# Kernel tuning notes

Hardware: AMD Instinct MI355X
Metric: run time of the kernel (lower is better)

Reference implementation:

```python
import jax, jax.numpy as jnp
import numpy as np

P = 8.0  # Lp norm order for NormDist layers (finite-p distance conv)
CHUNK = 8  # output-channel chunk for memory-bounded distance computation
EPS = 8.0 / 255.0


def lp_norm(d, p=P):
    # stable Lp norm over last axis: m * (sum((d/m)^p))^(1/p)
    m = jnp.max(d, axis=-1)
    ms = jnp.where(m > 0, m, 1.0)
    s = jnp.sum((d / ms[..., None]) ** p, axis=-1)
    ss = jnp.where(m > 0, s, 1.0)
    return m * ss ** (1.0 / p)


def extract_patches(t, k, s, pad):
    # [B,C,H,W] -> [B, L, C*k*k] (torch-unfold channel-major ordering), L=Ho*Wo
    pt = jax.lax.conv_general_dilated_patches(t, (k, k), (s, s), [(pad, pad), (pad, pad)])
    B, F, Ho, Wo = pt.shape
    return pt.reshape(B, F, Ho * Wo).transpose(0, 2, 1), Ho, Wo


def normdist_conv(c, lo, hi, w, k, s, pad):
    # Lp-distance conv with interval bound propagation on (center, lower, upper)
    pc, Ho, Wo = extract_patches(c, k, s, pad)
    pl, _, _ = extract_patches(lo, k, s, pad)
    ph, _, _ = extract_patches(hi, k, s, pad)
    O = w.shape[0]
    wf = w.reshape(O, -1)  # [O, F]

    def per_chunk(wc):  # wc: [CHUNK, F]
        dc = jnp.abs(pc[:, :, None, :] - wc)                     # [B,L,CHUNK,F]
        oc = lp_norm(dc)
        # per-element distance bounds given lo <= x <= hi
        dl = jnp.maximum(jnp.maximum(pl[:, :, None, :] - wc, wc - ph[:, :, None, :]), 0.0)
        ol = lp_norm(dl)
        dh = jnp.maximum(jnp.abs(pl[:, :, None, :] - wc), jnp.abs(ph[:, :, None, :] - wc))
        oh = lp_norm(dh)
        return oc, ol, oh

    oc, ol, oh = jax.lax.map(per_chunk, wf.reshape(O // CHUNK, CHUNK, -1))

    def to_img(t):  # [nch, B, L, CHUNK] -> [B, O, Ho, Wo]
        nch, B, L, ch = t.shape
        return t.transpose(1, 0, 3, 2).reshape(B, nch * ch, Ho, Wo)

    return to_img(oc), to_img(ol), to_img(oh)


def bound_relu(c, lo, hi):
    return jax.nn.relu(c), jax.nn.relu(lo), jax.nn.relu(hi)


def _mp(t):
    return jax.lax.reduce_window(t, -jnp.inf, jax.lax.max, (1, 1, 3, 3), (1, 1, 2, 2), 'VALID')


def bound_maxpool(c, lo, hi):
    return _mp(c), _mp(lo), _mp(hi)


def bound_linear(c, lo, hi, W, b=None):
    oc = c @ W.T
    mid = ((lo + hi) * 0.5) @ W.T
    rad = ((hi - lo) * 0.5) @ jnp.abs(W).T
    if b is not None:
        oc = oc + b
        mid = mid + b
    return oc, mid - rad, mid + rad


def setup_inputs() -> dict:
    key = jax.random.key(0)
    ks = jax.random.split(key, 10)
    x = jax.random.normal(ks[0], (16, 3, 32, 32), jnp.float32)
    lower = x - EPS
    upper = x + EPS
    w1 = jax.random.normal(ks[1], (96, 3, 7, 7), jnp.float32)
    w2 = jax.random.normal(ks[2], (256, 96, 5, 5), jnp.float32)
    w3 = jax.random.normal(ks[3], (384, 256, 3, 3), jnp.float32)
    w4 = jax.random.normal(ks[4], (384, 384, 3, 3), jnp.float32)
    w5 = jax.random.normal(ks[5], (256, 384, 3, 3), jnp.float32)
    fw1 = jax.random.normal(ks[6], (1024, 2304), jnp.float32) * 0.02
    fw2 = jax.random.normal(ks[7], (512, 1024), jnp.float32) * 0.03
    fw3 = jax.random.normal(ks[8], (10, 512), jnp.float32) * 0.04
    fb3 = jax.random.normal(ks[9], (10,), jnp.float32)
    return {"x": x, "lower": lower, "upper": upper, "w1": w1, "w2": w2, "w3": w3,
            "w4": w4, "w5": w5, "fw1": fw1, "fw2": fw2, "fw3": fw3, "fb3": fb3}


def reference(x, lower, upper, w1, w2, w3, w4, w5, fw1, fw2, fw3, fb3):
    c, l, u = normdist_conv(x, lower, upper, w1, 7, 2, 2)   # 32 -> 15
    c, l, u = bound_relu(c, l, u)
    c, l, u = bound_maxpool(c, l, u)                        # 15 -> 7
    c, l, u = normdist_conv(c, l, u, w2, 5, 1, 2)           # 7 -> 7
    c, l, u = bound_relu(c, l, u)
    c, l, u = bound_maxpool(c, l, u)                        # 7 -> 3
    c, l, u = normdist_conv(c, l, u, w3, 3, 1, 1)
    c, l, u = bound_relu(c, l, u)
    c, l, u = normdist_conv(c, l, u, w4, 3, 1, 1)
    c, l, u = bound_relu(c, l, u)
    c, l, u = normdist_conv(c, l, u, w5, 3, 1, 1)
    c, l, u = bound_relu(c, l, u)
    B = c.shape[0]
    c, l, u = c.reshape(B, -1), l.reshape(B, -1), u.reshape(B, -1)
    c, l, u = bound_linear(c, l, u, fw1)
    c, l, u = bound_relu(c, l, u)
    c, l, u = bound_linear(c, l, u, fw2)
    c, l, u = bound_relu(c, l, u)
    c, l, u = bound_linear(c, l, u, fw3, fb3)
    # final negation swaps the roles of lower/upper
    return (-c, -u, -l)
```

## Files before the change

kernel.cpp:

```cpp
#include <hip/hip_runtime.h>
#include <math.h>


typedef float vf2 __attribute__((ext_vector_type(2)));

__device__ __forceinline__ float rt8(float s) { return sqrtf(sqrtf(sqrtf(s))); }

__device__ __forceinline__ void tap16(float w, float pc, float pl, float pu,
                                      float& aC, float& aL, float& aH)
{
    float a = pc - w; float a2 = a * a, a4 = a2 * a2; aC = fmaf(a4, a4, aC);
    float x = pl - w, y = pu - w;
    float dl = fmaxf(fmaxf(x, -y), 0.f);
    float e2 = dl * dl, e4 = e2 * e2; aL = fmaf(e4, e4, aL);
    float h2 = fmaxf(x * x, y * y);
    float h4 = h2 * h2; aH = fmaf(h4, h4, aH);
}

__device__ __forceinline__ void tap16v2(vf2 w, vf2 pc, vf2 pl, vf2 pu,
                                        vf2& aC, vf2& aL, vf2& aH)
{
    vf2 a = pc - w; vf2 a2 = a * a, a4 = a2 * a2;
    aC = __builtin_elementwise_fma(a4, a4, aC);
    vf2 x = pl - w, y = pu - w;
    vf2 zero = {0.f, 0.f};
    vf2 dl = __builtin_elementwise_max(__builtin_elementwise_max(x, -y), zero);
    vf2 e2 = dl * dl, e4 = e2 * e2;
    aL = __builtin_elementwise_fma(e4, e4, aL);
    vf2 h2 = __builtin_elementwise_max(x * x, y * y);
    vf2 h4 = h2 * h2;
    aH = __builtin_elementwise_fma(h4, h4, aH);
}

__launch_bounds__(256)
__global__ void wtrans4(const float* __restrict__ W2, const float* __restrict__ W3,
                        const float* __restrict__ W4, const float* __restrict__ W5,
                        float* __restrict__ T2, float* __restrict__ T3,
                        float* __restrict__ T4, float* __restrict__ T5)
{
    constexpr int nt2 = 4 * 38, nt3 = 6 * 36, nt4 = 6 * 54, nt5 = 4 * 54;
    int bid = blockIdx.x;
    const float* W; float* T; int O, CK, KK, t;
    if (bid < nt2)                   { W = W2; T = T2; O = 256; CK = 2400; KK = 25; t = bid; }
    else if (bid < nt2 + nt3)        { W = W3; T = T3; O = 384; CK = 2304; KK = 9; t = bid - nt2; }
    else if (bid < nt2 + nt3 + nt4)  { W = W4; T = T4; O = 384; CK = 3456; KK = 9; t = bid - nt2 - nt3; }
    else                             { W = W5; T = T5; O = 256; CK = 3456; KK = 9; t = bid - nt2 - nt3 - nt4; }
    int tilesC = (CK + 63) / 64;
    int to = t / tilesC, tc = t - to * tilesC;
    int o0 = to * 64, c0 = tc * 64;
    __shared__ float tile[64][65];
    int lane = threadIdx.x & 63, wv = threadIdx.x >> 6;
    #pragma unroll
    for (int i = 0; i < 16; ++i) {
        int row = wv + i * 4;
        int c = c0 + lane;
        tile[row][lane] = (c < CK) ? W[(size_t)(o0 + row) * CK + c] : 0.f;
    }
    __syncthreads();
    #pragma unroll
    for (int i = 0; i < 16; ++i) {
        int row = wv + i * 4;
        int ck = c0 + row;
        if (ck < CK) {
            int c = ck / KK, tt = ck - c * KK;
            T[(size_t)((c >> 1) * KK + tt) * (2 * O) + (size_t)(o0 + lane) * 2 + (c & 1)]
                = tile[lane][row];
        }
    }
}

template<int K, int S, int PAD, int CC, int HIN, int WIN, int HO, int WO>
__launch_bounds__(256)
__global__ void conv_a(const float* __restrict__ IC, const float* __restrict__ IL,
                       const float* __restrict__ IU, const float* __restrict__ W,
                       float* __restrict__ OUT, int B, int Cin, int O, int OG)
{
    constexpr int PH = (HO - 1) * S + K;
    constexpr int PW = (WO - 1) * S + K;
    constexpr int PP = PH * PW;
    constexpr int HW = HIN * WIN;
    constexpr int NP = HO * WO;
    constexpr int ROUNDS = (NP + 63) / 64;
    __shared__ float lds[CC * 3 * PP];

    int og = blockIdx.x % OG;
    int b  = (blockIdx.x / OG) % B;
    int tid = threadIdx.x;

    for (int i = tid; i < CC * 3 * PP; i += 256) lds[i] = 0.f;
    __syncthreads();
    for (int tsel = 0; tsel < 3; ++tsel) {
        const float* src = (tsel == 0 ? IC : (tsel == 1 ? IL : IU))
                         + (size_t)b * Cin * HW;
        for (int e = tid; e < CC * HW; e += 256) {
            int c = e / HW, p = e % HW;
            int pr = p / WIN, pw_ = p % WIN;
            lds[c * 3 * PP + tsel * PP + (pr + PAD) * PW + (pw_ + PAD)] = src[e];
        }
    }
    __syncthreads();

    int wave = tid >> 6, lane = tid & 63;
    int o = __builtin_amdgcn_readfirstlane(og * 4 + wave);
    const float* wp = W + (size_t)o * Cin * (K * K);

    for (int r = 0; r < ROUNDS; ++r) {
        int pos = r * 64 + lane;
        bool act = pos < NP;
        int pp = act ? pos : 0;
        int oh = pp / WO, ow = pp % WO;
        const float* sl = lds + (oh * S) * PW + ow * S;
        const float* wc = wp;
        float aC = 0.f, aL = 0.f, aH = 0.f;
        for (int c = 0; c < CC; ++c) {
            #pragma unroll
            for (int kh = 0; kh < K; ++kh)
                #pragma unroll
                for (int kw = 0; kw < K; ++kw) {
                    float w = wc[kh * K + kw];
                    tap16(w, sl[kh * PW + kw], sl[PP + kh * PW + kw],
                          sl[2 * PP + kh * PW + kw], aC, aL, aH);
                }
            sl += 3 * PP; wc += K * K;
        }
        if (act) {
            size_t N = (size_t)B * O * NP;
            size_t oidx = ((size_t)b * O + o) * NP + pos;
            OUT[oidx] = aC; OUT[N + oidx] = aL; OUT[2 * N + oidx] = aH;
        }
    }
}

__global__ void pool_rt8(const float* __restrict__ in, float* __restrict__ out,
                         int BC, int Hin, int Win, int Ho, int Wo,
                         int n_in, int n_out)
{
    int idx = blockIdx.x * blockDim.x + threadIdx.x;
    int per = BC * Ho * Wo;
    if (idx >= 3 * per) return;
    int tsel = idx / per; int r = idx - tsel * per;
    int ow = r % Wo; int t2 = r / Wo;
    int oh = t2 % Ho; int bc = t2 / Ho;
    const float* ip = in + (size_t)tsel * n_in + (size_t)bc * Hin * Win;
    int ih0 = oh * 2, iw0 = ow * 2;
    float m = -INFINITY;
    #pragma unroll
    for (int i = 0; i < 3; ++i)
        #pragma unroll
        for (int j = 0; j < 3; ++j)
            m = fmaxf(m, ip[(ih0 + i) * Win + (iw0 + j)]);
    out[(size_t)tsel * n_out + r] = rt8(m);
}

template<int CC>
__launch_bounds__(256)
__global__ void conv2_kernel(const float* __restrict__ IN, const float* __restrict__ WT,
                             float* __restrict__ P, int nin)
{
    constexpr int B = 16, Cin = 96, O = 256;
    constexpr int CP = CC / 2;
    constexpr size_t N = (size_t)B * O * 49;
    __shared__ __align__(16) float slab[CP * 360];
    int x = blockIdx.x;
    int oh   = x % 7;
    int b    = (x / 7) % B;
    int chunk = x / (7 * B);
    int c0 = chunk * CC;
    int tid = threadIdx.x;

    for (int i = tid; i < CP * 360; i += 256) {
        int cp = i / 360; int rem = i - cp * 360;
        int tsel = rem / 120; int rr = rem - tsel * 120;
        int r = rr / 24; int cpar = rr - r * 24;
        int col = cpar >> 1, par = cpar & 1;
        int c = c0 + cp * 2 + par;
        int ih = oh + r - 2, iw = col - 2;
        float v = 0.f;
        if (col < 11 && (unsigned)ih < 7u && (unsigned)iw < 7u)
            v = IN[(size_t)tsel * nin + ((size_t)b * Cin + c) * 49 + ih * 7 + iw];
        slab[i] = v;
    }
    __syncthreads();

    int o = tid;
    vf2 aC2[7], aL2[7], aH2[7];
    vf2 zero = {0.f, 0.f};
    #pragma unroll
    for (int u = 0; u < 7; ++u) { aC2[u] = zero; aL2[u] = zero; aH2[u] = zero; }

    for (int cp = 0; cp < CP; ++cp) {
        const float* wp = WT + (size_t)((c0 / 2 + cp) * 25) * (2 * O) + 2 * o;
        const float* sb = slab + cp * 360;
        #pragma unroll
        for (int r = 0; r < 5; ++r) {
            vf2 wr[5];
            #pragma unroll
            for (int kw = 0; kw < 5; ++kw)
                wr[kw] = *(const vf2*)(wp + (size_t)(r * 5 + kw) * (2 * O));
            vf2 X[12], L[12], U[12];
            #pragma unroll
            for (int i2 = 0; i2 < 12; ++i2) {
                X[i2] = *(const vf2*)(sb + r * 24 + i2 * 2);
                L[i2] = *(const vf2*)(sb + 120 + r * 24 + i2 * 2);
                U[i2] = *(const vf2*)(sb + 240 + r * 24 + i2 * 2);
            }
            #pragma unroll
            for (int ow = 0; ow < 7; ++ow)
                #pragma unroll
                for (int kw = 0; kw < 5; ++kw)
                    tap16v2(wr[kw], X[ow + kw], L[ow + kw], U[ow + kw],
                            aC2[ow], aL2[ow], aH2[ow]);
        }
    }

    float* Pc = P + (size_t)chunk * 3 * N;
    size_t rowbase = ((size_t)(b * 7 + oh) * 7) * O + o;
    #pragma unroll
    for (int u = 0; u < 7; ++u) {
        Pc[rowbase + (size_t)u * O]         = aC2[u].x + aC2[u].y;
        Pc[N + rowbase + (size_t)u * O]     = aL2[u].x + aL2[u].y;
        Pc[2 * N + rowbase + (size_t)u * O] = aH2[u].x + aH2[u].y;
    }
}

__global__ void comb2_pool2(const float* __restrict__ P, float* __restrict__ D)
{
    constexpr int B = 16, O = 256, NCH = 16;
    constexpr size_t N = (size_t)B * O * 49;
    int idx = blockIdx.x * blockDim.x + threadIdx.x;
    if (idx >= 3 * B * 9 * O) return;
    int o = idx & 255; int t = idx >> 8;
    int pos = t % 9; t /= 9;
    int b = t % B; int tsel = t / B;
    int ph = pos / 3, pw = pos % 3;
    float m = 0.f;
    #pragma unroll
    for (int i = 0; i < 3; ++i)
        #pragma unroll
        for (int j = 0; j < 3; ++j) {
            int sp = (ph * 2 + i) * 7 + (pw * 2 + j);
            size_t base = (size_t)tsel * N + ((size_t)b * 49 + sp) * O + o;
            float s = 0.f;
            #pragma unroll
            for (int ch = 0; ch < NCH; ++ch) s += P[(size_t)ch * 3 * N + base];
            m = fmaxf(m, s);
        }
    D[idx] = rt8(m);
}

template<int CC>
__launch_bounds__(384)
__global__ void conv3x3_kernel(const float* __restrict__ IN, const float* __restrict__ WT,
                               float* __restrict__ P, int B, int Cin, int O)
{
    constexpr int CP = CC / 2;
    __shared__ __align__(8) float slab[CP * 150];
    int x = blockIdx.x;
    int b = x % B;
    int chunk = x / B;
    int c0 = chunk * CC;
    int tid = threadIdx.x;

    for (int i = tid; i < CP * 150; i += blockDim.x) {
        int cp = i / 150; int rem = i - cp * 150;
        int tsel = rem / 50; int rr = rem - tsel * 50;
        int p = rr >> 1, par = rr & 1;
        int iy = p / 5, ix = p - iy * 5;
        int ih = iy - 1, iw = ix - 1;
        int c = c0 + cp * 2 + par;
        float v = 0.f;
        if ((unsigned)ih < 3u && (unsigned)iw < 3u)
            v = IN[(((size_t)tsel * B + b) * 9 + (ih * 3 + iw)) * Cin + c];
        slab[i] = v;
    }
    __syncthreads();

    int o = tid;
    vf2 aC2[9], aL2[9], aH2[9];
    vf2 zero = {0.f, 0.f};
    #pragma unroll
    for (int u = 0; u < 9; ++u) { aC2[u] = zero; aL2[u] = zero; aH2[u] = zero; }

    for (int cp = 0; cp < CP; ++cp) {
        const float* wp = WT + (size_t)((c0 / 2 + cp) * 9) * (2 * O) + 2 * o;
        vf2 w2[9];
        #pragma unroll
        for (int t = 0; t < 9; ++t) w2[t] = *(const vf2*)(wp + (size_t)t * (2 * O));
        const float* sb = slab + cp * 150;
        #pragma unroll
        for (int py = 0; py < 3; ++py)
            #pragma unroll
            for (int px = 0; px < 3; ++px)
                #pragma unroll
                for (int ky = 0; ky < 3; ++ky)
                    #pragma unroll
                    for (int kx = 0; kx < 3; ++kx) {
                        int p = (py + ky) * 5 + (px + kx);
                        tap16v2(w2[ky * 3 + kx],
                                *(const vf2*)(sb + p * 2),
                                *(const vf2*)(sb + 50 + p * 2),
                                *(const vf2*)(sb + 100 + p * 2),
                                aC2[py * 3 + px], aL2[py * 3 + px], aH2[py * 3 + px]);
                    }
    }

    size_t N = (size_t)B * O * 9;
    float* Pc = P + (size_t)chunk * 3 * N;
    size_t base = ((size_t)b * 9) * O + o;
    #pragma unroll
    for (int u = 0; u < 9; ++u) {
        Pc[base + (size_t)u * O]         = aC2[u].x + aC2[u].y;
        Pc[N + base + (size_t)u * O]     = aL2[u].x + aL2[u].y;
        Pc[2 * N + base + (size_t)u * O] = aH2[u].x + aH2[u].y;
    }
}

__global__ void conv_comb_flat(const float* __restrict__ P, float* __restrict__ OUT,
                               size_t N3, int NCH)
{
    size_t idx = (size_t)blockIdx.x * blockDim.x + threadIdx.x;
    if (idx >= N3) return;
    float s = 0.f;
    for (int ch = 0; ch < NCH; ++ch) s += P[(size_t)ch * N3 + idx];
    OUT[idx] = rt8(s);
}

__global__ void comb5_std(const float* __restrict__ P, float* __restrict__ G, int NCH)
{
    constexpr int B = 16, O = 256;
    constexpr size_t N = (size_t)B * O * 9;
    size_t idx = (size_t)blockIdx.x * blockDim.x + threadIdx.x;
    if (idx >= 3 * N) return;
    float s = 0.f;
    for (int ch = 0; ch < NCH; ++ch) s += P[(size_t)ch * 3 * N + idx];
    int o = (int)(idx % O); size_t t = idx / O;
    int pos = (int)(t % 9); t /= 9;
    int b = (int)(t % B); int tsel = (int)(t / B);
    G[(size_t)tsel * N + ((size_t)b * O + o) * 9 + pos] = rt8(s);
}

__launch_bounds__(256)
__global__ void fc_gemv(const float* __restrict__ IC, const float* __restrict__ IL,
                        const float* __restrict__ IU, const float* __restrict__ W,
                        float* __restrict__ OUT, int B, int In, int Out)
{
    int gw = (int)((blockIdx.x * blockDim.x + threadIdx.x) >> 6);
    int lane = threadIdx.x & 63;
    if (gw >= B * Out) return;
    int o = gw % Out, b = gw / Out;
    const float4* wr = (const float4*)(W  + (size_t)o * In);
    const float4* cr = (const float4*)(IC + (size_t)b * In);
    const float4* lr = (const float4*)(IL + (size_t)b * In);
    const float4* ur = (const float4*)(IU + (size_t)b * In);
    int In4 = In >> 2;
    float sc = 0.f, sm = 0.f, sr = 0.f;
    for (int i = lane; i < In4; i += 64) {
        float4 w4 = wr[i], c4 = cr[i], l4 = lr[i], u4 = ur[i];
        sc = fmaf(c4.x, w4.x, sc); sc = fmaf(c4.y, w4.y, sc);
        sc = fmaf(c4.z, w4.z, sc); sc = fmaf(c4.w, w4.w, sc);
        sm = fmaf((l4.x + u4.x) * 0.5f, w4.x, sm);
        sm = fmaf((l4.y + u4.y) * 0.5f, w4.y, sm);
        sm = fmaf((l4.z + u4.z) * 0.5f, w4.z, sm);
        sm = fmaf((l4.w + u4.w) * 0.5f, w4.w, sm);
        sr = fmaf((u4.x - l4.x) * 0.5f, fabsf(w4.x), sr);
        sr = fmaf((u4.y - l4.y) * 0.5f, fabsf(w4.y), sr);
        sr = fmaf((u4.z - l4.z) * 0.5f, fabsf(w4.z), sr);
        sr = fmaf((u4.w - l4.w) * 0.5f, fabsf(w4.w), sr);
    }
    #pragma unroll
    for (int off = 32; off; off >>= 1) {
        sc += __shfl_xor(sc, off);
        sm += __shfl_xor(sm, off);
        sr += __shfl_xor(sr, off);
    }
    if (lane == 0) {
        size_t N = (size_t)B * Out;
        size_t idx = (size_t)b * Out + o;
        OUT[idx]         = fmaxf(sc, 0.f);
        OUT[N + idx]     = fmaxf(sm - sr, 0.f);
        OUT[2 * N + idx] = fmaxf(sm + sr, 0.f);
    }
}

__global__ void bound_linear_kernel(
    const float* __restrict__ IC, const float* __restrict__ IL, const float* __restrict__ IU,
    const float* __restrict__ W, const float* __restrict__ bias,
    float* __restrict__ OC, float* __restrict__ OL, float* __restrict__ OU,
    int B, int In, int Out)
{
    int idx = blockIdx.x * blockDim.x + threadIdx.x;
    if (idx >= B * Out) return;
    int o = idx % Out, b = idx / Out;
    const float* wr = W  + (size_t)o * In;
    const float* cr = IC + (size_t)b * In;
    const float* lr = IL + (size_t)b * In;
    const float* ur = IU + (size_t)b * In;
    float sc = 0.f, sm = 0.f, sr = 0.f;
    for (int i = 0; i < In; ++i) {
        float w = wr[i];
        sc = fmaf(cr[i], w, sc);
        sm = fmaf((lr[i] + ur[i]) * 0.5f, w, sm);
        sr = fmaf((ur[i] - lr[i]) * 0.5f, fabsf(w), sr);
    }
    float bb = bias[o]; sc += bb; sm += bb;
    OC[idx] = -sc; OL[idx] = -(sm - sr); OU[idx] = -(sm + sr);
}

extern "C" void kernel_launch(void* const* d_in, const int* in_sizes, int n_in,
                              void* d_out, int out_size, void* d_ws, size_t ws_size,
                              hipStream_t stream)
{
    const float* x   = (const float*)d_in[0];
    const float* lo  = (const float*)d_in[1];
    const float* hi  = (const float*)d_in[2];
    const float* w1  = (const float*)d_in[3];
    const float* w2  = (const float*)d_in[4];
    const float* w3  = (const float*)d_in[5];
    const float* w4  = (const float*)d_in[6];
    const float* w5  = (const float*)d_in[7];
    const float* fw1 = (const float*)d_in[8];
    const float* fw2 = (const float*)d_in[9];
    const float* fw3 = (const float*)d_in[10];
    const float* fb3 = (const float*)d_in[11];
    float* out = (float*)d_out;
    float* ws  = (float*)d_ws;

    const size_t n_c1 = 16u * 96 * 15 * 15;
    const size_t n_p1 = 16u * 96 * 7 * 7;
    const size_t n_d  = 16u * 256 * 9;
    const size_t n_c3 = 16u * 384 * 9;
    const size_t n_c5 = 16u * 256 * 9;
    const size_t n_f1 = 16u * 1024;
    const size_t n_f2 = 16u * 512;

    float* A   = ws;
    float* Bp  = A  + 3 * n_c1;
    float* D   = Bp + 3 * n_p1;
    float* E   = D  + 3 * n_d;
    float* F   = E  + 3 * n_c3;
    float* G   = F  + 3 * n_c3;
    float* H   = G  + 3 * n_c5;
    float* I   = H  + 3 * n_f1;
    float* WT2 = I  + 3 * n_f2;
    float* WT3 = WT2 + 614400;
    float* WT4 = WT3 + 884736;
    float* WT5 = WT4 + 1327104;
    float* SP  = WT5 + 884736;

    const int BS = 256;
    auto grid = [](size_t tot) { return dim3((unsigned)((tot + 255) / 256)); };

    wtrans4<<<4 * 38 + 6 * 36 + 6 * 54 + 4 * 54, BS, 0, stream>>>(
        w2, w3, w4, w5, WT2, WT3, WT4, WT5);

    conv_a<7, 2, 2, 3, 32, 32, 15, 15><<<384, BS, 0, stream>>>(
        x, lo, hi, w1, A, 16, 3, 96, 24);
    pool_rt8<<<grid(3 * n_p1), BS, 0, stream>>>(
        A, Bp, 16 * 96, 15, 15, 7, 7, (int)n_c1, (int)n_p1);
    conv2_kernel<6><<<16 * 16 * 7, 256, 0, stream>>>(Bp, WT2, SP, (int)n_p1);
    comb2_pool2<<<grid(3 * n_d), BS, 0, stream>>>(SP, D);
    conv3x3_kernel<8><<<32 * 16, 384, 0, stream>>>(D, WT3, SP, 16, 256, 384);
    conv_comb_flat<<<grid(3 * n_c3), BS, 0, stream>>>(SP, E, 3 * n_c3, 32);
    conv3x3_kernel<8><<<48 * 16, 384, 0, stream>>>(E, WT4, SP, 16, 384, 384);
    conv_comb_flat<<<grid(3 * n_c3), BS, 0, stream>>>(SP, F, 3 * n_c3, 48);
    conv3x3_kernel<8><<<48 * 16, 256, 0, stream>>>(F, WT5, SP, 16, 384, 256);
    comb5_std<<<grid(3 * n_c5), BS, 0, stream>>>(SP, G, 48);
    fc_gemv<<<grid(16384u * 64), BS, 0, stream>>>(
        G, G + n_c5, G + 2 * n_c5, fw1, H, 16, 2304, 1024);
    fc_gemv<<<grid(8192u * 64), BS, 0, stream>>>(
        H, H + n_f1, H + 2 * n_f1, fw2, I, 16, 1024, 512);
    bound_linear_kernel<<<grid(160), BS, 0, stream>>>(
        I, I + n_f2, I + 2 * n_f2, fw3, fb3,
        out, out + 320, out + 160, 16, 512, 10);
}
```

Measured before the change: 593.6 us.

## Fuse weight transpose with conv1, and fold pooling and partial-sum reductions into consumers

New measurement: 582.5 us. No clear change (-1.9%).

```diff
diff --git a/kernel.cpp b/kernel.cpp
--- a/kernel.cpp
+++ b/kernel.cpp
@@ -33,133 +33,102 @@
 }
 
 __launch_bounds__(256)
-__global__ void wtrans4(const float* __restrict__ W2, const float* __restrict__ W3,
-                        const float* __restrict__ W4, const float* __restrict__ W5,
-                        float* __restrict__ T2, float* __restrict__ T3,
-                        float* __restrict__ T4, float* __restrict__ T5)
-{
-    constexpr int nt2 = 4 * 38, nt3 = 6 * 36, nt4 = 6 * 54, nt5 = 4 * 54;
+__global__ void prep_kernel(const float* __restrict__ W2, const float* __restrict__ W3,
+                            const float* __restrict__ W4, const float* __restrict__ W5,
+                            float* __restrict__ T2, float* __restrict__ T3,
+                            float* __restrict__ T4, float* __restrict__ T5,
+                            const float* __restrict__ IC, const float* __restrict__ IL,
+                            const float* __restrict__ IU, const float* __restrict__ W1,
+                            float* __restrict__ A)
+{
+    constexpr int nt2 = 152, nt3 = 216, nt4 = 324, nt5 = 216;
+    constexpr int NTW = nt2 + nt3 + nt4 + nt5;
+    __shared__ float u[3 * 3 * 1225];
     int bid = blockIdx.x;
-    const float* W; float* T; int O, CK, KK, t;
-    if (bid < nt2)                   { W = W2; T = T2; O = 256; CK = 2400; KK = 25; t = bid; }
-    else if (bid < nt2 + nt3)        { W = W3; T = T3; O = 384; CK = 2304; KK = 9; t = bid - nt2; }
-    else if (bid < nt2 + nt3 + nt4)  { W = W4; T = T4; O = 384; CK = 3456; KK = 9; t = bid - nt2 - nt3; }
-    else                             { W = W5; T = T5; O = 256; CK = 3456; KK = 9; t = bid - nt2 - nt3 - nt4; }
-    int tilesC = (CK + 63) / 64;
-    int to = t / tilesC, tc = t - to * tilesC;
-    int o0 = to * 64, c0 = tc * 64;
-    __shared__ float tile[64][65];
-    int lane = threadIdx.x & 63, wv = threadIdx.x >> 6;
-    #pragma unroll
-    for (int i = 0; i < 16; ++i) {
-        int row = wv + i * 4;
-        int c = c0 + lane;
-        tile[row][lane] = (c < CK) ? W[(size_t)(o0 + row) * CK + c] : 0.f;
-    }
-    __syncthreads();
-    #pragma unroll
-    for (int i = 0; i < 16; ++i) {
-        int row = wv + i * 4;
-        int ck = c0 + row;
-        if (ck < CK) {
-            int c = ck / KK, tt = ck - c * KK;
-            T[(size_t)((c >> 1) * KK + tt) * (2 * O) + (size_t)(o0 + lane) * 2 + (c & 1)]
-                = tile[lane][row];
-        }
-    }
-}
-
-template<int K, int S, int PAD, int CC, int HIN, int WIN, int HO, int WO>
-__launch_bounds__(256)
-__global__ void conv_a(const float* __restrict__ IC, const float* __restrict__ IL,
-                       const float* __restrict__ IU, const float* __restrict__ W,
-                       float* __restrict__ OUT, int B, int Cin, int O, int OG)
-{
-    constexpr int PH = (HO - 1) * S + K;
-    constexpr int PW = (WO - 1) * S + K;
-    constexpr int PP = PH * PW;
-    constexpr int HW = HIN * WIN;
-    constexpr int NP = HO * WO;
-    constexpr int ROUNDS = (NP + 63) / 64;
-    __shared__ float lds[CC * 3 * PP];
-
-    int og = blockIdx.x % OG;
-    int b  = (blockIdx.x / OG) % B;
     int tid = threadIdx.x;
 
-    for (int i = tid; i < CC * 3 * PP; i += 256) lds[i] = 0.f;
+    if (bid < NTW) {
+        const float* W; float* T; int O, CK, KK, t;
+        if (bid < nt2)                  { W = W2; T = T2; O = 256; CK = 2400; KK = 25; t = bid; }
+        else if (bid < nt2 + nt3)       { W = W3; T = T3; O = 384; CK = 2304; KK = 9; t = bid - nt2; }
+        else if (bid < nt2 + nt3 + nt4) { W = W4; T = T4; O = 384; CK = 3456; KK = 9; t = bid - nt2 - nt3; }
+        else                            { W = W5; T = T5; O = 256; CK = 3456; KK = 9; t = bid - nt2 - nt3 - nt4; }
+        int tilesC = (CK + 63) / 64;
+        int to = t / tilesC, tc = t - to * tilesC;
+        int o0 = to * 64, c0 = tc * 64;
+        int lane = tid & 63, wv = tid >> 6;
+        #pragma unroll
+        for (int i = 0; i < 16; ++i) {
+            int row = wv + i * 4;
+            int c = c0 + lane;
+            u[row * 65 + lane] = (c < CK) ? W[(size_t)(o0 + row) * CK + c] : 0.f;
+        }
+        __syncthreads();
+        #pragma unroll
+        for (int i = 0; i < 16; ++i) {
+            int row = wv + i * 4;
+            int ck = c0 + row;
+            if (ck < CK) {
+                int c = ck / KK, tt = ck - c * KK;
+                T[(size_t)((c >> 1) * KK + tt) * (2 * O) + (size_t)(o0 + lane) * 2 + (c & 1)]
+                    = u[lane * 65 + row];
+            }
+        }
+        return;
+    }
+
+    constexpr int PP = 1225, PW = 35, HW = 1024;
+    int t = bid - NTW;
+    int og = t % 24; t /= 24;
+    int b  = t % 16; int r = t / 16;
+
+    for (int i = tid; i < 3 * 3 * PP; i += 256) u[i] = 0.f;
     __syncthreads();
     for (int tsel = 0; tsel < 3; ++tsel) {
-        const float* src = (tsel == 0 ? IC : (tsel == 1 ? IL : IU))
-                         + (size_t)b * Cin * HW;
-        for (int e = tid; e < CC * HW; e += 256) {
+        const float* src = (tsel == 0 ? IC : (tsel == 1 ? IL : IU)) + (size_t)b * 3 * HW;
+        for (int e = tid; e < 3 * HW; e += 256) {
             int c = e / HW, p = e % HW;
-            int pr = p / WIN, pw_ = p % WIN;
-            lds[c * 3 * PP + tsel * PP + (pr + PAD) * PW + (pw_ + PAD)] = src[e];
+            int pr = p / 32, pw_ = p % 32;
+            u[c * 3 * PP + tsel * PP + (pr + 2) * PW + (pw_ + 2)] = src[e];
         }
     }
     __syncthreads();
 
     int wave = tid >> 6, lane = tid & 63;
-    int o = __builtin_amdgcn_readfirstlane(og * 4 + wave);
-    const float* wp = W + (size_t)o * Cin * (K * K);
-
-    for (int r = 0; r < ROUNDS; ++r) {
-        int pos = r * 64 + lane;
-        bool act = pos < NP;
-        int pp = act ? pos : 0;
-        int oh = pp / WO, ow = pp % WO;
-        const float* sl = lds + (oh * S) * PW + ow * S;
-        const float* wc = wp;
+    int o = og * 4 + wave;
+    const float* wp = W1 + (size_t)o * 147;
+    int pos = r * 64 + lane;
+    if (pos < 225) {
+        int oh = pos / 15, ow = pos % 15;
+        const float* sl = u + (oh * 2) * PW + ow * 2;
         float aC = 0.f, aL = 0.f, aH = 0.f;
-        for (int c = 0; c < CC; ++c) {
-            #pragma unroll
-            for (int kh = 0; kh < K; ++kh)
+        #pragma unroll
+        for (int c = 0; c < 3; ++c) {
+            #pragma unroll
+            for (int kh = 0; kh < 7; ++kh)
                 #pragma unroll
-                for (int kw = 0; kw < K; ++kw) {
-                    float w = wc[kh * K + kw];
+                for (int kw = 0; kw < 7; ++kw) {
+                    float w = wp[c * 49 + kh * 7 + kw];
                     tap16(w, sl[kh * PW + kw], sl[PP + kh * PW + kw],
                           sl[2 * PP + kh * PW + kw], aC, aL, aH);
                 }
-            sl += 3 * PP; wc += K * K;
-        }
-        if (act) {
-            size_t N = (size_t)B * O * NP;
-            size_t oidx = ((size_t)b * O + o) * NP + pos;
-            OUT[oidx] = aC; OUT[N + oidx] = aL; OUT[2 * N + oidx] = aH;
-        }
-    }
-}
-
-__global__ void pool_rt8(const float* __restrict__ in, float* __restrict__ out,
-                         int BC, int Hin, int Win, int Ho, int Wo,
-                         int n_in, int n_out)
-{
-    int idx = blockIdx.x * blockDim.x + threadIdx.x;
-    int per = BC * Ho * Wo;
-    if (idx >= 3 * per) return;
-    int tsel = idx / per; int r = idx - tsel * per;
-    int ow = r % Wo; int t2 = r / Wo;
-    int oh = t2 % Ho; int bc = t2 / Ho;
-    const float* ip = in + (size_t)tsel * n_in + (size_t)bc * Hin * Win;
-    int ih0 = oh * 2, iw0 = ow * 2;
-    float m = -INFINITY;
-    #pragma unroll
-    for (int i = 0; i < 3; ++i)
-        #pragma unroll
-        for (int j = 0; j < 3; ++j)
-            m = fmaxf(m, ip[(ih0 + i) * Win + (iw0 + j)]);
-    out[(size_t)tsel * n_out + r] = rt8(m);
+            sl += 3 * PP;
+        }
+        size_t N = (size_t)16 * 96 * 225;
+        size_t oi = ((size_t)b * 96 + o) * 225 + pos;
+        A[oi] = aC; A[N + oi] = aL; A[2 * N + oi] = aH;
+    }
 }
 
 template<int CC>
 __launch_bounds__(256)
-__global__ void conv2_kernel(const float* __restrict__ IN, const float* __restrict__ WT,
-                             float* __restrict__ P, int nin)
+__global__ void conv2_kernel(const float* __restrict__ A, const float* __restrict__ WT,
+                             float* __restrict__ P)
 {
     constexpr int B = 16, Cin = 96, O = 256;
     constexpr int CP = CC / 2;
     constexpr size_t N = (size_t)B * O * 49;
+    constexpr size_t NA = (size_t)B * 96 * 225;
     __shared__ __align__(16) float slab[CP * 360];
     int x = blockIdx.x;
     int oh   = x % 7;
@@ -176,8 +145,17 @@
         int c = c0 + cp * 2 + par;
         int ih = oh + r - 2, iw = col - 2;
         float v = 0.f;
-        if (col < 11 && (unsigned)ih < 7u && (unsigned)iw < 7u)
-            v = IN[(size_t)tsel * nin + ((size_t)b * Cin + c) * 49 + ih * 7 + iw];
+        if (col < 11 && (unsigned)ih < 7u && (unsigned)iw < 7u) {
+            const float* ap = A + (size_t)tsel * NA + ((size_t)b * 96 + c) * 225
+                            + (ih * 2) * 15 + iw * 2;
+            float m = 0.f;
+            #pragma unroll
+            for (int pi = 0; pi < 3; ++pi)
+                #pragma unroll
+                for (int pj = 0; pj < 3; ++pj)
+                    m = fmaxf(m, ap[pi * 15 + pj]);
+            v = rt8(m);
+        }
         slab[i] = v;
     }
     __syncthreads();
@@ -248,7 +226,7 @@
     D[idx] = rt8(m);
 }
 
-template<int CC>
+template<int CC, int NCHIN>
 __launch_bounds__(384)
 __global__ void conv3x3_kernel(const float* __restrict__ IN, const float* __restrict__ WT,
                                float* __restrict__ P, int B, int Cin, int O)
@@ -261,6 +239,7 @@
     int c0 = chunk * CC;
     int tid = threadIdx.x;
 
+    size_t NN = (size_t)B * Cin * 9;
     for (int i = tid; i < CP * 150; i += blockDim.x) {
         int cp = i / 150; int rem = i - cp * 150;
         int tsel = rem / 50; int rr = rem - tsel * 50;
@@ -269,8 +248,17 @@
         int ih = iy - 1, iw = ix - 1;
         int c = c0 + cp * 2 + par;
         float v = 0.f;
-        if ((unsigned)ih < 3u && (unsigned)iw < 3u)
-            v = IN[(((size_t)tsel * B + b) * 9 + (ih * 3 + iw)) * Cin + c];
+        if ((unsigned)ih < 3u && (unsigned)iw < 3u) {
+            size_t base = (size_t)tsel * NN + ((size_t)b * 9 + (ih * 3 + iw)) * Cin + c;
+            if (NCHIN == 0) {
+                v = IN[base];
+            } else {
+                float s = 0.f;
+                #pragma unroll 8
+                for (int ch = 0; ch < NCHIN; ++ch) s += IN[(size_t)ch * 3 * NN + base];
+                v = rt8(s);
+            }
+        }
         slab[i] = v;
     }
     __syncthreads();
@@ -313,16 +301,6 @@
         Pc[N + base + (size_t)u * O]     = aL2[u].x + aL2[u].y;
         Pc[2 * N + base + (size_t)u * O] = aH2[u].x + aH2[u].y;
     }
-}
-
-__global__ void conv_comb_flat(const float* __restrict__ P, float* __restrict__ OUT,
-                               size_t N3, int NCH)
-{
-    size_t idx = (size_t)blockIdx.x * blockDim.x + threadIdx.x;
-    if (idx >= N3) return;
-    float s = 0.f;
-    for (int ch = 0; ch < NCH; ++ch) s += P[(size_t)ch * N3 + idx];
-    OUT[idx] = rt8(s);
 }
 
 __global__ void comb5_std(const float* __restrict__ P, float* __restrict__ G, int NCH)
@@ -425,46 +403,38 @@
     float* out = (float*)d_out;
     float* ws  = (float*)d_ws;
 
-    const size_t n_c1 = 16u * 96 * 15 * 15;
-    const size_t n_p1 = 16u * 96 * 7 * 7;
+    const size_t n_c1 = 16u * 96 * 225;
     const size_t n_d  = 16u * 256 * 9;
-    const size_t n_c3 = 16u * 384 * 9;
     const size_t n_c5 = 16u * 256 * 9;
     const size_t n_f1 = 16u * 1024;
     const size_t n_f2 = 16u * 512;
+    const size_t N3   = 16u * 384 * 9;
 
     float* A   = ws;
-    float* Bp  = A  + 3 * n_c1;
-    float* D   = Bp + 3 * n_p1;
-    float* E   = D  + 3 * n_d;
-    float* F   = E  + 3 * n_c3;
-    float* G   = F  + 3 * n_c3;
+    float* D   = A  + 3 * n_c1;
+    float* G   = D  + 3 * n_d;
     float* H   = G  + 3 * n_c5;
     float* I   = H  + 3 * n_f1;
     float* WT2 = I  + 3 * n_f2;
     float* WT3 = WT2 + 614400;
     float* WT4 = WT3 + 884736;
     float* WT5 = WT4 + 1327104;
-    float* SP  = WT5 + 884736;
+    float* SP2 = WT5 + 884736;
+    float* SPa = SP2;
+    float* SPc = SP2;
+    float* SPb = SP2 + 32u * 3 * N3;
 
     const int BS = 256;
     auto grid = [](size_t tot) { return dim3((unsigned)((tot + 255) / 256)); };
 
-    wtrans4<<<4 * 38 + 6 * 36 + 6 * 54 + 4 * 54, BS, 0, stream>>>(
-        w2, w3, w4, w5, WT2, WT3, WT4, WT5);
-
-    conv_a<7, 2, 2, 3, 32, 32, 15, 15><<<384, BS, 0, stream>>>(
-        x, lo, hi, w1, A, 16, 3, 96, 24);
-    pool_rt8<<<grid(3 * n_p1), BS, 0, stream>>>(
-        A, Bp, 16 * 96, 15, 15, 7, 7, (int)n_c1, (int)n_p1);
-    conv2_kernel<6><<<16 * 16 * 7, 256, 0, stream>>>(Bp, WT2, SP, (int)n_p1);
-    comb2_pool2<<<grid(3 * n_d), BS, 0, stream>>>(SP, D);
-    conv3x3_kernel<8><<<32 * 16, 384, 0, stream>>>(D, WT3, SP, 16, 256, 384);
-    conv_comb_flat<<<grid(3 * n_c3), BS, 0, stream>>>(SP, E, 3 * n_c3, 32);
-    conv3x3_kernel<8><<<48 * 16, 384, 0, stream>>>(E, WT4, SP, 16, 384, 384);
-    conv_comb_flat<<<grid(3 * n_c3), BS, 0, stream>>>(SP, F, 3 * n_c3, 48);
-    conv3x3_kernel<8><<<48 * 16, 256, 0, stream>>>(F, WT5, SP, 16, 384, 256);
-    comb5_std<<<grid(3 * n_c5), BS, 0, stream>>>(SP, G, 48);
+    prep_kernel<<<908 + 1536, BS, 0, stream>>>(
+        w2, w3, w4, w5, WT2, WT3, WT4, WT5, x, lo, hi, w1, A);
+    conv2_kernel<6><<<16 * 16 * 7, 256, 0, stream>>>(A, WT2, SP2);
+    comb2_pool2<<<grid(3 * n_d), BS, 0, stream>>>(SP2, D);
+    conv3x3_kernel<8, 0><<<32 * 16, 384, 0, stream>>>(D, WT3, SPa, 16, 256, 384);
+    conv3x3_kernel<8, 32><<<48 * 16, 384, 0, stream>>>(SPa, WT4, SPb, 16, 384, 384);
+    conv3x3_kernel<8, 48><<<48 * 16, 256, 0, stream>>>(SPb, WT5, SPc, 16, 384, 256);
+    comb5_std<<<grid(3 * n_c5), BS, 0, stream>>>(SPc, G, 48);
     fc_gemv<<<grid(16384u * 64), BS, 0, stream>>>(
         G, G + n_c5, G + 2 * n_c5, fw1, H, 16, 2304, 1024);
     fc_gemv<<<grid(8192u * 64), BS, 0, stream>>>(
```
